# Kernel tuning notes

Measured on AMD Instinct MI355X. Metric: run time of the kernel, lower is better.

Reference implementation:

```python
import jax, jax.numpy as jnp
import numpy as np
from jax import lax

BN_EPS = 1e-5


def _conv(x, w, b):
    # 3x3 conv, stride 1, padding 1 (SAME), NCHW/OIHW
    y = lax.conv_general_dilated(x, w, (1, 1), 'SAME',
                                 dimension_numbers=('NCHW', 'OIHW', 'NCHW'))
    return y + b[None, :, None, None]


def _bn(x, g, b, m, v):
    # eval-mode batchnorm with running stats
    scale = (g / jnp.sqrt(v + BN_EPS))[None, :, None, None]
    return (x - m[None, :, None, None]) * scale + b[None, :, None, None]


def _pool(x):
    # MaxPool2d(2,2), VALID (floor division of spatial dims)
    return lax.reduce_window(x, -jnp.inf, lax.max, (1, 1, 2, 2), (1, 1, 2, 2), 'VALID')


def _quantum(xq, qp):
    """Batched 5-qubit statevector sim of the PennyLane circuit.
    Wire i: RX(xq[:, i%2]) then RY(qp[i%2]); CNOT(0,1); CNOT(1,2); <Z0 Z1>.
    xq: [B, 32] (only first 2 features used). Returns [B] float32.
    """
    B = xq.shape[0]
    psi = jnp.zeros((B, 32), jnp.complex64).at[:, 0].set(1.0)
    for i in range(5):  # fixed tiny loop over wires
        a = xq[:, i % 2]          # [B] data angle
        th = qp[i % 2]            # scalar weight angle
        ca, sa = jnp.cos(a * 0.5), jnp.sin(a * 0.5)
        RX = jnp.stack([jnp.stack([ca, -1j * sa], -1),
                        jnp.stack([-1j * sa, ca], -1)], -2).astype(jnp.complex64)  # [B,2,2]
        cb, sb = jnp.cos(th * 0.5), jnp.sin(th * 0.5)
        RY = jnp.stack([jnp.stack([cb, -sb]), jnp.stack([sb, cb])]).astype(jnp.complex64)  # [2,2]
        U = jnp.einsum('ij,bjk->bik', RY, RX)  # [B,2,2] per-wire unitary
        psi = psi.reshape(B, 2 ** i, 2, 2 ** (4 - i))
        psi = jnp.einsum('bij,bajc->baic', U, psi).reshape(B, 32)
    psi = psi.reshape(B, 2, 2, 2, 2, 2)
    # CNOT(0,1): flip qubit 1 where qubit 0 == 1
    psi = psi.at[:, 1].set(psi[:, 1, ::-1])
    # CNOT(1,2): flip qubit 2 where qubit 1 == 1
    psi = psi.at[:, :, 1].set(psi[:, :, 1, ::-1])
    z01 = jnp.array([[1.0, -1.0], [-1.0, 1.0]], jnp.float32).reshape(1, 2, 2, 1, 1, 1)
    prob = jnp.real(psi) ** 2 + jnp.imag(psi) ** 2
    return jnp.sum(prob * z01, axis=(1, 2, 3, 4, 5))


def setup_inputs() -> dict:
    key = jax.random.key(0)
    ks = jax.random.split(key, 24)
    B = 8192
    s = 0.05
    d = {}
    d['x'] = jax.random.normal(ks[0], (B, 1, 28, 28), jnp.float32)
    d['conv1_w'] = jax.random.normal(ks[1], (64, 1, 3, 3), jnp.float32) * s
    d['conv1_b'] = jax.random.normal(ks[2], (64,), jnp.float32) * s
    d['conv2_w'] = jax.random.normal(ks[3], (128, 64, 3, 3), jnp.float32) * s
    d['conv2_b'] = jax.random.normal(ks[4], (128,), jnp.float32) * s
    d['conv3_w'] = jax.random.normal(ks[5], (256, 128, 3, 3), jnp.float32) * s
    d['conv3_b'] = jax.random.normal(ks[6], (256,), jnp.float32) * s
    for i, c in [(1, 64), (2, 128), (3, 256)]:
        d[f'bn{i}_g'] = jnp.ones((c,), jnp.float32)
        d[f'bn{i}_b'] = jnp.zeros((c,), jnp.float32)
        d[f'bn{i}_m'] = jax.random.normal(ks[6 + i], (c,), jnp.float32) * 0.1
        d[f'bn{i}_v'] = jax.random.uniform(ks[9 + i], (c,), jnp.float32, 0.5, 1.5)
    d['fc1_w'] = jax.random.normal(ks[13], (32, 256 * 3 * 3), jnp.float32) * s
    d['fc1_b'] = jax.random.normal(ks[14], (32,), jnp.float32) * s
    d['q_params'] = jax.random.uniform(ks[15], (8,), jnp.float32)
    d['fc2_w'] = jax.random.normal(ks[16], (128, 1), jnp.float32) * s
    d['fc2_b'] = jax.random.normal(ks[17], (128,), jnp.float32) * s
    d['fc3_w'] = jax.random.normal(ks[18], (2, 128), jnp.float32) * s
    d['fc3_b'] = jax.random.normal(ks[19], (2,), jnp.float32) * s
    return d


def reference(x, conv1_w, conv1_b, conv2_w, conv2_b, conv3_w, conv3_b,
              bn1_g, bn1_b, bn1_m, bn1_v, bn2_g, bn2_b, bn2_m, bn2_v,
              bn3_g, bn3_b, bn3_m, bn3_v, fc1_w, fc1_b, q_params,
              fc2_w, fc2_b, fc3_w, fc3_b):
    h = _pool(jax.nn.relu(_bn(_conv(x, conv1_w, conv1_b), bn1_g, bn1_b, bn1_m, bn1_v)))
    h = _pool(jax.nn.relu(_bn(_conv(h, conv2_w, conv2_b), bn2_g, bn2_b, bn2_m, bn2_v)))
    h = _pool(jax.nn.relu(_bn(_conv(h, conv3_w, conv3_b), bn3_g, bn3_b, bn3_m, bn3_v)))
    # dropout is identity in eval mode
    h = h.reshape(h.shape[0], -1)              # [B, 2304]
    h = h @ fc1_w.T + fc1_b                     # [B, 32]
    q = _quantum(h, q_params)[:, None]          # [B, 1]
    h = q @ fc2_w.T + fc2_b                     # [B, 128]
    logits = h @ fc3_w.T + fc3_b                # [B, 2]
    return jax.nn.log_softmax(logits, axis=1)
```

## Files before the change

### kernel.cpp

```cpp
#include <hip/hip_runtime.h>
#include <hip/hip_bf16.h>
#include <math.h>

typedef float f32x4 __attribute__((ext_vector_type(4)));
typedef short s16x8 __attribute__((ext_vector_type(8)));

static const long long OFF_W2  = 0LL;
static const long long OFF_W3  = 147456LL;
static const long long OFF_AB1 = 737280LL;
static const long long OFF_AB2 = 737792LL;
static const long long OFF_AB3 = 738816LL;
static const long long OFF_Q   = 740864LL;

__device__ inline unsigned short f2bfu(float f) {
    __hip_bfloat16 h = __float2bfloat16(f);
    unsigned short u;
    __builtin_memcpy(&u, &h, 2);
    return u;
}

__global__ __launch_bounds__(256) void prep_k(
    const float* __restrict__ c2w, const float* __restrict__ c3w,
    const float* __restrict__ c1b, const float* __restrict__ g1, const float* __restrict__ b1,
    const float* __restrict__ m1, const float* __restrict__ v1,
    const float* __restrict__ c2b, const float* __restrict__ g2, const float* __restrict__ b2,
    const float* __restrict__ m2, const float* __restrict__ v2,
    const float* __restrict__ c3b, const float* __restrict__ g3, const float* __restrict__ b3,
    const float* __restrict__ m3, const float* __restrict__ v3,
    const float* __restrict__ fc1b, const float* __restrict__ qp,
    const float* __restrict__ fc2w, const float* __restrict__ fc2b,
    const float* __restrict__ fc3w, const float* __restrict__ fc3b,
    short* __restrict__ wT2, short* __restrict__ wT3,
    float2* __restrict__ ab1, float2* __restrict__ ab2, float2* __restrict__ ab3,
    float* __restrict__ qc)
{
    int tid = blockIdx.x * 256 + threadIdx.x;
    if (tid < 73728) {
        int ic = tid & 63, oc = (tid >> 6) & 127, k = tid >> 13;
        wT2[tid] = (short)f2bfu(c2w[(oc * 64 + ic) * 9 + k]);
    }
    if (tid < 294912) {
        int ic = tid & 127, oc = (tid >> 7) & 255, k = tid >> 15;
        wT3[tid] = (short)f2bfu(c3w[(oc * 128 + ic) * 9 + k]);
    }
    if (tid < 64) {
        float s = g1[tid] / sqrtf(v1[tid] + 1e-5f);
        ab1[tid] = make_float2(s, (c1b[tid] - m1[tid]) * s + b1[tid]);
    } else if (tid < 192) {
        int c = tid - 64;
        float s = g2[c] / sqrtf(v2[c] + 1e-5f);
        ab2[c] = make_float2(s, (c2b[c] - m2[c]) * s + b2[c]);
    } else if (tid < 448) {
        int c = tid - 192;
        float s = g3[c] / sqrtf(v3[c] + 1e-5f);
        ab3[c] = make_float2(s, (c3b[c] - m3[c]) * s + b3[c]);
    } else if (tid == 448) {
        float A0 = 0.f, A1 = 0.f, B0 = 0.f, B1 = 0.f;
        for (int k = 0; k < 128; ++k) {
            float f2 = fc2w[k], fb = fc2b[k];
            A0 += fc3w[k] * f2;        B0 += fc3w[k] * fb;
            A1 += fc3w[128 + k] * f2;  B1 += fc3w[128 + k] * fb;
        }
        qc[0] = A0; qc[1] = A1;
        qc[2] = B0 + fc3b[0]; qc[3] = B1 + fc3b[1];
        qc[4] = cosf(qp[1]);  qc[5] = fc1b[1];
    }
}

__global__ __launch_bounds__(256, 2) void fused_k(
    const float* __restrict__ x, const float* __restrict__ c1w,
    const float2* __restrict__ ab1, const float2* __restrict__ ab2,
    const float2* __restrict__ ab3,
    const short* __restrict__ wT2, const short* __restrict__ wT3,
    const float* __restrict__ fc1w, const float* __restrict__ qc,
    float* __restrict__ out)
{
    __shared__ float xt[30][32];
    __shared__ short xs2[16 * 16 * 64];
    __shared__ short xs3[8 * 8 * 128];
    __shared__ float red[4];

    int b = blockIdx.x, t = threadIdx.x;

    for (int i = t; i < 960;  i += 256) ((float*)xt)[i] = 0.f;
    for (int i = t; i < 8192; i += 256) ((unsigned*)xs2)[i] = 0u;
    for (int i = t; i < 4096; i += 256) ((unsigned*)xs3)[i] = 0u;
    __syncthreads();

    for (int i = t; i < 784; i += 256) xt[i / 28 + 1][i % 28 + 1] = x[b * 784 + i];

    int ocg = t & 7;
    float wr[8][9];
    float2 abr[8];
#pragma unroll
    for (int c = 0; c < 8; ++c) {
#pragma unroll
        for (int k = 0; k < 9; ++k) wr[c][k] = c1w[(ocg * 8 + c) * 9 + k];
        abr[c] = ab1[ocg * 8 + c];
    }
    __syncthreads();

    int posb = t >> 3;
    for (int p = posb; p < 196; p += 32) {
        int py = p / 14, px = p % 14;
        int y0 = 2 * py, x0 = 2 * px;
        float patch[4][4];
#pragma unroll
        for (int i = 0; i < 4; ++i)
#pragma unroll
            for (int j = 0; j < 4; ++j) patch[i][j] = xt[y0 + i][x0 + j];

        unsigned short ub[8];
#pragma unroll
        for (int c = 0; c < 8; ++c) {
            float a00 = 0.f, a01 = 0.f, a10 = 0.f, a11 = 0.f;
#pragma unroll
            for (int ky = 0; ky < 3; ++ky)
#pragma unroll
                for (int kx = 0; kx < 3; ++kx) {
                    float wv = wr[c][ky * 3 + kx];
                    a00 += patch[ky + 0][kx + 0] * wv;
                    a01 += patch[ky + 0][kx + 1] * wv;
                    a10 += patch[ky + 1][kx + 0] * wv;
                    a11 += patch[ky + 1][kx + 1] * wv;
                }
            float aa = abr[c].x, bb = abr[c].y;
            float v = fmaxf(fmaxf(a00 * aa + bb, a01 * aa + bb),
                            fmaxf(a10 * aa + bb, a11 * aa + bb));
            ub[c] = f2bfu(fmaxf(v, 0.f));
        }
        uint4 pk;
        pk.x = (unsigned)ub[0] | ((unsigned)ub[1] << 16);
        pk.y = (unsigned)ub[2] | ((unsigned)ub[3] << 16);
        pk.z = (unsigned)ub[4] | ((unsigned)ub[5] << 16);
        pk.w = (unsigned)ub[6] | ((unsigned)ub[7] << 16);
        int blk = ocg ^ ((px + 1) & 7);
        *(uint4*)&xs2[((((py + 1) * 16) + (px + 1)) * 8 + blk) * 8] = pk;
    }
    __syncthreads();

    int lane = t & 63, wid = t >> 6;
    int quad = lane >> 4, n16 = lane & 15;
    int dy = n16 >> 3, lx = n16 & 7;

    {
        f32x4 acc0[14], acc1[14];
        f32x4 z = {0.f, 0.f, 0.f, 0.f};
#pragma unroll
        for (int nt = 0; nt < 14; ++nt) { acc0[nt] = z; acc1[nt] = z; }

#pragma unroll 1
        for (int kykx = 0; kykx < 9; ++kykx) {
            int ky = kykx / 3, kx = kykx - 3 * ky;
            int dyky = dy + ky;
            int xc0 = lx + kx;
            int xc1 = xc0 + 8; if (xc1 > 15) xc1 = 15;
#pragma unroll
            for (int kk = 0; kk < 2; ++kk) {
                s16x8 A0 = *(const s16x8*)(wT2 + ((kykx * 128 + (wid * 2 + 0) * 16 + n16) * 64 + kk * 32 + quad * 8));
                s16x8 A1 = *(const s16x8*)(wT2 + ((kykx * 128 + (wid * 2 + 1) * 16 + n16) * 64 + kk * 32 + quad * 8));
                int bi = kk * 4 + quad;
#pragma unroll
                for (int nt = 0; nt < 14; ++nt) {
                    int ry = nt >> 1, cb = nt & 1;
                    int y_in = 2 * ry + dyky;
                    int x_in = cb ? xc1 : xc0;
                    int blk = bi ^ (x_in & 7);
                    s16x8 B = *(const s16x8*)&xs2[((y_in * 16 + x_in) * 8 + blk) * 8];
                    acc0[nt] = __builtin_amdgcn_mfma_f32_16x16x32_bf16(A0, B, acc0[nt], 0, 0, 0);
                    acc1[nt] = __builtin_amdgcn_mfma_f32_16x16x32_bf16(A1, B, acc1[nt], 0, 0, 0);
                }
            }
        }

        int m = lx >> 1;
        bool keep = (dy == 0) && ((lx & 1) == 0);
#pragma unroll
        for (int ml = 0; ml < 2; ++ml) {
            int oc0 = (wid * 2 + ml) * 16 + quad * 4;
            float2 abv[4];
#pragma unroll
            for (int r = 0; r < 4; ++r) abv[r] = ab2[oc0 + r];
#pragma unroll
            for (int nt = 0; nt < 14; ++nt) {
                int ry = nt >> 1, cb = nt & 1;
                int xp = cb * 4 + m;
                float pv[4];
#pragma unroll
                for (int r = 0; r < 4; ++r) {
                    float v = (ml ? acc1[nt][r] : acc0[nt][r]) * abv[r].x + abv[r].y;
                    v = fmaxf(v, __shfl_xor(v, 1));
                    v = fmaxf(v, __shfl_xor(v, 8));
                    pv[r] = fmaxf(v, 0.f);
                }
                if (keep && xp < 7) {
                    uint2 pk;
                    pk.x = (unsigned)f2bfu(pv[0]) | ((unsigned)f2bfu(pv[1]) << 16);
                    pk.y = (unsigned)f2bfu(pv[2]) | ((unsigned)f2bfu(pv[3]) << 16);
                    int blk3 = (oc0 >> 3) ^ (((xp + 1) & 7) << 1);
                    *(uint2*)&xs3[(((ry + 1) * 8 + (xp + 1)) * 16 + blk3) * 8 + (oc0 & 7)] = pk;
                }
            }
        }
    }
    __syncthreads();

    f32x4 acc[4][3];
    f32x4 z = {0.f, 0.f, 0.f, 0.f};
#pragma unroll
    for (int ml = 0; ml < 4; ++ml)
#pragma unroll
        for (int nt = 0; nt < 3; ++nt) acc[ml][nt] = z;

#pragma unroll 1
    for (int kykx = 0; kykx < 9; ++kykx) {
        int ky = kykx / 3, kx = kykx - 3 * ky;
        int dyky = dy + ky;
        int x_in = lx + kx; if (x_in > 7) x_in = 7;
#pragma unroll
        for (int kk = 0; kk < 4; ++kk) {
            s16x8 A[4];
#pragma unroll
            for (int ml = 0; ml < 4; ++ml)
                A[ml] = *(const s16x8*)(wT3 + ((kykx * 256 + (wid * 4 + ml) * 16 + n16) * 128 + kk * 32 + quad * 8));
            int bi = kk * 4 + quad;
            int blk = bi ^ ((x_in & 7) << 1);
#pragma unroll
            for (int nt = 0; nt < 3; ++nt) {
                int y_in = 2 * nt + dyky;
                s16x8 B = *(const s16x8*)&xs3[((y_in * 8 + x_in) * 16 + blk) * 8];
#pragma unroll
                for (int ml = 0; ml < 4; ++ml)
                    acc[ml][nt] = __builtin_amdgcn_mfma_f32_16x16x32_bf16(A[ml], B, acc[ml][nt], 0, 0, 0);
            }
        }
    }

    float vacc = 0.f;
    int m = lx >> 1;
    bool keep = (dy == 0) && ((lx & 1) == 0) && (m < 3);
    const float* fc1w1 = fc1w + 2304;
#pragma unroll
    for (int ml = 0; ml < 4; ++ml) {
        int oc0 = (wid * 4 + ml) * 16 + quad * 4;
        float2 abv[4];
#pragma unroll
        for (int r = 0; r < 4; ++r) abv[r] = ab3[oc0 + r];
#pragma unroll
        for (int nt = 0; nt < 3; ++nt) {
#pragma unroll
            for (int r = 0; r < 4; ++r) {
                float v = acc[ml][nt][r] * abv[r].x + abv[r].y;
                v = fmaxf(v, __shfl_xor(v, 1));
                v = fmaxf(v, __shfl_xor(v, 8));
                v = fmaxf(v, 0.f);
                if (keep) vacc += v * fc1w1[(oc0 + r) * 9 + nt * 3 + m];
            }
        }
    }
#pragma unroll
    for (int s = 1; s < 64; s <<= 1) vacc += __shfl_xor(vacc, s);
    if (lane == 0) red[wid] = vacc;
    __syncthreads();
    if (t == 0) {
        float v = red[0] + red[1] + red[2] + red[3] + qc[5];
        float q = cosf(v) * qc[4];
        float l0 = q * qc[0] + qc[2];
        float l1 = q * qc[1] + qc[3];
        float mx = fmaxf(l0, l1);
        float lse = mx + logf(__expf(l0 - mx) + __expf(l1 - mx));
        out[b * 2 + 0] = l0 - lse;
        out[b * 2 + 1] = l1 - lse;
    }
}

extern "C" void kernel_launch(void* const* d_in, const int* in_sizes, int n_in,
                              void* d_out, int out_size, void* d_ws, size_t ws_size,
                              hipStream_t stream)
{
    const float* x    = (const float*)d_in[0];
    const float* c1w  = (const float*)d_in[1];
    const float* c1b  = (const float*)d_in[2];
    const float* c2w  = (const float*)d_in[3];
    const float* c2b  = (const float*)d_in[4];
    const float* c3w  = (const float*)d_in[5];
    const float* c3b  = (const float*)d_in[6];
    const float* g1   = (const float*)d_in[7];
    const float* b1   = (const float*)d_in[8];
    const float* m1   = (const float*)d_in[9];
    const float* v1   = (const float*)d_in[10];
    const float* g2   = (const float*)d_in[11];
    const float* b2   = (const float*)d_in[12];
    const float* m2   = (const float*)d_in[13];
    const float* v2   = (const float*)d_in[14];
    const float* g3   = (const float*)d_in[15];
    const float* b3   = (const float*)d_in[16];
    const float* m3   = (const float*)d_in[17];
    const float* v3   = (const float*)d_in[18];
    const float* fc1w = (const float*)d_in[19];
    const float* fc1b = (const float*)d_in[20];
    const float* qp   = (const float*)d_in[21];
    const float* fc2w = (const float*)d_in[22];
    const float* fc2b = (const float*)d_in[23];
    const float* fc3w = (const float*)d_in[24];
    const float* fc3b = (const float*)d_in[25];
    float* out = (float*)d_out;
    char* ws = (char*)d_ws;

    short*  wT2 = (short*)(ws + OFF_W2);
    short*  wT3 = (short*)(ws + OFF_W3);
    float2* ab1 = (float2*)(ws + OFF_AB1);
    float2* ab2 = (float2*)(ws + OFF_AB2);
    float2* ab3 = (float2*)(ws + OFF_AB3);
    float*  qc  = (float*)(ws + OFF_Q);

    int B = in_sizes[0] / 784;

    prep_k<<<1152, 256, 0, stream>>>(c2w, c3w, c1b, g1, b1, m1, v1,
                                     c2b, g2, b2, m2, v2, c3b, g3, b3, m3, v3,
                                     fc1b, qp, fc2w, fc2b, fc3w, fc3b,
                                     wT2, wT3, ab1, ab2, ab3, qc);
    fused_k<<<B, 256, 0, stream>>>(x, c1w, ab1, ab2, ab3, wT2, wT3, fc1w, qc, out);
}
```

Measured before the change: 987.2 us.

## Alias conv2/conv3 LDS buffers, retile MFMA work per wave, raise occupancy

Merges the conv2 and conv3 LDS staging buffers into one aliased buffer that is re-zeroed between stages, cutting shared memory per block so launch bounds can request 3 blocks per SM. Conv2 is retiled so each wave owns one column half and 64 output channels, reusing 4 A fragments across 7 B loads. Conv3 is split by output-channel half and row group, which leaves an uneven 2-vs-1 tile split between waves. Conv1 uses packed float2 math. The risks are register pressure from the tighter bound and load imbalance in conv3.

Result: slower. 2.219 ms (+124.7%).

```diff
diff --git a/kernel.cpp b/kernel.cpp
--- a/kernel.cpp
+++ b/kernel.cpp
@@ -4,6 +4,7 @@
 
 typedef float f32x4 __attribute__((ext_vector_type(4)));
 typedef short s16x8 __attribute__((ext_vector_type(8)));
+typedef float v2f   __attribute__((ext_vector_type(2)));
 
 static const long long OFF_W2  = 0LL;
 static const long long OFF_W3  = 147456LL;
@@ -67,7 +68,7 @@
     }
 }
 
-__global__ __launch_bounds__(256, 2) void fused_k(
+__global__ __launch_bounds__(256, 3) void fused_k(
     const float* __restrict__ x, const float* __restrict__ c1w,
     const float2* __restrict__ ab1, const float2* __restrict__ ab2,
     const float2* __restrict__ ab3,
@@ -75,16 +76,14 @@
     const float* __restrict__ fc1w, const float* __restrict__ qc,
     float* __restrict__ out)
 {
+    __shared__ short smem[16 * 16 * 64 + 128];
     __shared__ float xt[30][32];
-    __shared__ short xs2[16 * 16 * 64];
-    __shared__ short xs3[8 * 8 * 128];
     __shared__ float red[4];
 
     int b = blockIdx.x, t = threadIdx.x;
 
+    for (int i = t; i < 8256; i += 256) ((unsigned*)smem)[i] = 0u;
     for (int i = t; i < 960;  i += 256) ((float*)xt)[i] = 0.f;
-    for (int i = t; i < 8192; i += 256) ((unsigned*)xs2)[i] = 0u;
-    for (int i = t; i < 4096; i += 256) ((unsigned*)xs3)[i] = 0u;
     __syncthreads();
 
     for (int i = t; i < 784; i += 256) xt[i / 28 + 1][i % 28 + 1] = x[b * 784 + i];
@@ -104,30 +103,31 @@
     for (int p = posb; p < 196; p += 32) {
         int py = p / 14, px = p % 14;
         int y0 = 2 * py, x0 = 2 * px;
-        float patch[4][4];
-#pragma unroll
-        for (int i = 0; i < 4; ++i)
-#pragma unroll
-            for (int j = 0; j < 4; ++j) patch[i][j] = xt[y0 + i][x0 + j];
-
+        v2f rowv[4][2];
+#pragma unroll
+        for (int i = 0; i < 4; ++i) {
+            rowv[i][0] = *(const v2f*)&xt[y0 + i][x0];
+            rowv[i][1] = *(const v2f*)&xt[y0 + i][x0 + 2];
+        }
         unsigned short ub[8];
 #pragma unroll
         for (int c = 0; c < 8; ++c) {
-            float a00 = 0.f, a01 = 0.f, a10 = 0.f, a11 = 0.f;
-#pragma unroll
-            for (int ky = 0; ky < 3; ++ky)
-#pragma unroll
-                for (int kx = 0; kx < 3; ++kx) {
-                    float wv = wr[c][ky * 3 + kx];
-                    a00 += patch[ky + 0][kx + 0] * wv;
-                    a01 += patch[ky + 0][kx + 1] * wv;
-                    a10 += patch[ky + 1][kx + 0] * wv;
-                    a11 += patch[ky + 1][kx + 1] * wv;
-                }
+            v2f a0 = {0.f, 0.f}, a1 = {0.f, 0.f};
+#pragma unroll
+            for (int ky = 0; ky < 3; ++ky) {
+                float w0 = wr[c][ky * 3 + 0], w1 = wr[c][ky * 3 + 1], w2 = wr[c][ky * 3 + 2];
+                v2f p00 = rowv[ky][0],     p01 = rowv[ky][1];
+                v2f p10 = rowv[ky + 1][0], p11 = rowv[ky + 1][1];
+                v2f q0; q0.x = p00.y; q0.y = p01.x;
+                v2f q1; q1.x = p10.y; q1.y = p11.x;
+                a0 += p00 * w0; a0 += q0 * w1; a0 += p01 * w2;
+                a1 += p10 * w0; a1 += q1 * w1; a1 += p11 * w2;
+            }
             float aa = abr[c].x, bb = abr[c].y;
-            float v = fmaxf(fmaxf(a00 * aa + bb, a01 * aa + bb),
-                            fmaxf(a10 * aa + bb, a11 * aa + bb));
-            ub[c] = f2bfu(fmaxf(v, 0.f));
+            v2f r0 = a0 * aa + bb;
+            v2f r1 = a1 * aa + bb;
+            float v = fmaxf(fmaxf(fmaxf(r0.x, r0.y), fmaxf(r1.x, r1.y)), 0.f);
+            ub[c] = f2bfu(v);
         }
         uint4 pk;
         pk.x = (unsigned)ub[0] | ((unsigned)ub[1] << 16);
@@ -135,126 +135,157 @@
         pk.z = (unsigned)ub[4] | ((unsigned)ub[5] << 16);
         pk.w = (unsigned)ub[6] | ((unsigned)ub[7] << 16);
         int blk = ocg ^ ((px + 1) & 7);
-        *(uint4*)&xs2[((((py + 1) * 16) + (px + 1)) * 8 + blk) * 8] = pk;
+        *(uint4*)&smem[((((py + 1) * 16) + (px + 1)) * 8 + blk) * 8] = pk;
     }
     __syncthreads();
 
     int lane = t & 63, wid = t >> 6;
     int quad = lane >> 4, n16 = lane & 15;
     int dy = n16 >> 3, lx = n16 & 7;
+    int cb = wid >> 1;
+    int oh = wid & 1;
 
     {
-        f32x4 acc0[14], acc1[14];
+        f32x4 acc[4][7];
         f32x4 z = {0.f, 0.f, 0.f, 0.f};
 #pragma unroll
-        for (int nt = 0; nt < 14; ++nt) { acc0[nt] = z; acc1[nt] = z; }
+        for (int ml = 0; ml < 4; ++ml)
+#pragma unroll
+            for (int ry = 0; ry < 7; ++ry) acc[ml][ry] = z;
 
 #pragma unroll 1
         for (int kykx = 0; kykx < 9; ++kykx) {
             int ky = kykx / 3, kx = kykx - 3 * ky;
-            int dyky = dy + ky;
-            int xc0 = lx + kx;
-            int xc1 = xc0 + 8; if (xc1 > 15) xc1 = 15;
+            int y0 = dy + ky;
+            int xc = lx + kx + cb * 8;
+            const short* aB = wT2 + (kykx * 128 + oh * 64 + n16) * 64 + quad * 8;
 #pragma unroll
             for (int kk = 0; kk < 2; ++kk) {
-                s16x8 A0 = *(const s16x8*)(wT2 + ((kykx * 128 + (wid * 2 + 0) * 16 + n16) * 64 + kk * 32 + quad * 8));
-                s16x8 A1 = *(const s16x8*)(wT2 + ((kykx * 128 + (wid * 2 + 1) * 16 + n16) * 64 + kk * 32 + quad * 8));
-                int bi = kk * 4 + quad;
-#pragma unroll
-                for (int nt = 0; nt < 14; ++nt) {
-                    int ry = nt >> 1, cb = nt & 1;
-                    int y_in = 2 * ry + dyky;
-                    int x_in = cb ? xc1 : xc0;
-                    int blk = bi ^ (x_in & 7);
-                    s16x8 B = *(const s16x8*)&xs2[((y_in * 16 + x_in) * 8 + blk) * 8];
-                    acc0[nt] = __builtin_amdgcn_mfma_f32_16x16x32_bf16(A0, B, acc0[nt], 0, 0, 0);
-                    acc1[nt] = __builtin_amdgcn_mfma_f32_16x16x32_bf16(A1, B, acc1[nt], 0, 0, 0);
-                }
-            }
-        }
+                int blk = (kk * 4 + quad) ^ (xc & 7);
+                const short* bp = &smem[((y0 * 16 + xc) * 8 + blk) * 8];
+                s16x8 A[4];
+#pragma unroll
+                for (int ml = 0; ml < 4; ++ml)
+                    A[ml] = *(const s16x8*)(aB + ml * 1024 + kk * 32);
+#pragma unroll
+                for (int ry = 0; ry < 7; ++ry) {
+                    s16x8 B = *(const s16x8*)(bp + ry * 2048);
+#pragma unroll
+                    for (int ml = 0; ml < 4; ++ml)
+                        acc[ml][ry] = __builtin_amdgcn_mfma_f32_16x16x32_bf16(A[ml], B, acc[ml][ry], 0, 0, 0);
+                }
+            }
+        }
+
+        __syncthreads();
+        for (int i = t; i < 4224; i += 256) ((unsigned*)smem)[i] = 0u;
+        __syncthreads();
 
         int m = lx >> 1;
-        bool keep = (dy == 0) && ((lx & 1) == 0);
-#pragma unroll
-        for (int ml = 0; ml < 2; ++ml) {
-            int oc0 = (wid * 2 + ml) * 16 + quad * 4;
+        int xp = cb * 4 + m;
+        bool keep = (dy == 0) && ((lx & 1) == 0) && (xp < 7);
+#pragma unroll
+        for (int ml = 0; ml < 4; ++ml) {
+            int oc0 = oh * 64 + ml * 16 + quad * 4;
             float2 abv[4];
 #pragma unroll
             for (int r = 0; r < 4; ++r) abv[r] = ab2[oc0 + r];
 #pragma unroll
-            for (int nt = 0; nt < 14; ++nt) {
-                int ry = nt >> 1, cb = nt & 1;
-                int xp = cb * 4 + m;
+            for (int ry = 0; ry < 7; ++ry) {
                 float pv[4];
 #pragma unroll
                 for (int r = 0; r < 4; ++r) {
-                    float v = (ml ? acc1[nt][r] : acc0[nt][r]) * abv[r].x + abv[r].y;
+                    float v = acc[ml][ry][r] * abv[r].x + abv[r].y;
                     v = fmaxf(v, __shfl_xor(v, 1));
                     v = fmaxf(v, __shfl_xor(v, 8));
                     pv[r] = fmaxf(v, 0.f);
                 }
-                if (keep && xp < 7) {
+                if (keep) {
                     uint2 pk;
                     pk.x = (unsigned)f2bfu(pv[0]) | ((unsigned)f2bfu(pv[1]) << 16);
                     pk.y = (unsigned)f2bfu(pv[2]) | ((unsigned)f2bfu(pv[3]) << 16);
                     int blk3 = (oc0 >> 3) ^ (((xp + 1) & 7) << 1);
-                    *(uint2*)&xs3[(((ry + 1) * 8 + (xp + 1)) * 16 + blk3) * 8 + (oc0 & 7)] = pk;
-                }
-            }
-        }
-    }
-    __syncthreads();
-
-    f32x4 acc[4][3];
-    f32x4 z = {0.f, 0.f, 0.f, 0.f};
-#pragma unroll
-    for (int ml = 0; ml < 4; ++ml)
-#pragma unroll
-        for (int nt = 0; nt < 3; ++nt) acc[ml][nt] = z;
-
+                    *(uint2*)&smem[(((ry + 1) * 8 + (xp + 1)) * 16 + blk3) * 8 + (oc0 & 7)] = pk;
+                }
+            }
+        }
+    }
+    __syncthreads();
+
+    int oh3 = wid & 1;
+    int nth = wid >> 1;
+
+    f32x4 acc3[8][2];
+    {
+        f32x4 z = {0.f, 0.f, 0.f, 0.f};
+#pragma unroll
+        for (int ml = 0; ml < 8; ++ml) { acc3[ml][0] = z; acc3[ml][1] = z; }
+    }
+
+    if (nth == 0) {
 #pragma unroll 1
-    for (int kykx = 0; kykx < 9; ++kykx) {
-        int ky = kykx / 3, kx = kykx - 3 * ky;
-        int dyky = dy + ky;
-        int x_in = lx + kx; if (x_in > 7) x_in = 7;
-#pragma unroll
-        for (int kk = 0; kk < 4; ++kk) {
-            s16x8 A[4];
-#pragma unroll
-            for (int ml = 0; ml < 4; ++ml)
-                A[ml] = *(const s16x8*)(wT3 + ((kykx * 256 + (wid * 4 + ml) * 16 + n16) * 128 + kk * 32 + quad * 8));
-            int bi = kk * 4 + quad;
-            int blk = bi ^ ((x_in & 7) << 1);
-#pragma unroll
-            for (int nt = 0; nt < 3; ++nt) {
-                int y_in = 2 * nt + dyky;
-                s16x8 B = *(const s16x8*)&xs3[((y_in * 8 + x_in) * 16 + blk) * 8];
-#pragma unroll
-                for (int ml = 0; ml < 4; ++ml)
-                    acc[ml][nt] = __builtin_amdgcn_mfma_f32_16x16x32_bf16(A[ml], B, acc[ml][nt], 0, 0, 0);
+        for (int kykx = 0; kykx < 9; ++kykx) {
+            int ky = kykx / 3, kx = kykx - 3 * ky;
+            int y0 = dy + ky;
+            int x0 = lx + kx;
+            const short* aB = wT3 + (kykx * 256 + oh3 * 128 + n16) * 128 + quad * 8;
+#pragma unroll
+            for (int kk = 0; kk < 4; ++kk) {
+                int blk = (kk * 4 + quad) ^ ((x0 & 7) << 1);
+                const short* bp = &smem[((y0 * 8 + x0) * 16 + blk) * 8];
+                s16x8 B0 = *(const s16x8*)(bp);
+                s16x8 B1 = *(const s16x8*)(bp + 2048);
+#pragma unroll
+                for (int ml = 0; ml < 8; ++ml) {
+                    s16x8 A = *(const s16x8*)(aB + ml * 2048 + kk * 32);
+                    acc3[ml][0] = __builtin_amdgcn_mfma_f32_16x16x32_bf16(A, B0, acc3[ml][0], 0, 0, 0);
+                    acc3[ml][1] = __builtin_amdgcn_mfma_f32_16x16x32_bf16(A, B1, acc3[ml][1], 0, 0, 0);
+                }
+            }
+        }
+    } else {
+#pragma unroll 1
+        for (int kykx = 0; kykx < 9; ++kykx) {
+            int ky = kykx / 3, kx = kykx - 3 * ky;
+            int y0 = dy + ky;
+            int x0 = lx + kx;
+            const short* aB = wT3 + (kykx * 256 + oh3 * 128 + n16) * 128 + quad * 8;
+#pragma unroll
+            for (int kk = 0; kk < 4; ++kk) {
+                int blk = (kk * 4 + quad) ^ ((x0 & 7) << 1);
+                const short* bp = &smem[((y0 * 8 + x0) * 16 + blk) * 8 + 4096];
+                s16x8 B0 = *(const s16x8*)(bp);
+#pragma unroll
+                for (int ml = 0; ml < 8; ++ml) {
+                    s16x8 A = *(const s16x8*)(aB + ml * 2048 + kk * 32);
+                    acc3[ml][0] = __builtin_amdgcn_mfma_f32_16x16x32_bf16(A, B0, acc3[ml][0], 0, 0, 0);
+                }
             }
         }
     }
 
     float vacc = 0.f;
-    int m = lx >> 1;
-    bool keep = (dy == 0) && ((lx & 1) == 0) && (m < 3);
-    const float* fc1w1 = fc1w + 2304;
-#pragma unroll
-    for (int ml = 0; ml < 4; ++ml) {
-        int oc0 = (wid * 4 + ml) * 16 + quad * 4;
-        float2 abv[4];
-#pragma unroll
-        for (int r = 0; r < 4; ++r) abv[r] = ab3[oc0 + r];
-#pragma unroll
-        for (int nt = 0; nt < 3; ++nt) {
-#pragma unroll
-            for (int r = 0; r < 4; ++r) {
-                float v = acc[ml][nt][r] * abv[r].x + abv[r].y;
-                v = fmaxf(v, __shfl_xor(v, 1));
-                v = fmaxf(v, __shfl_xor(v, 8));
-                v = fmaxf(v, 0.f);
-                if (keep) vacc += v * fc1w1[(oc0 + r) * 9 + nt * 3 + m];
+    {
+        int m = lx >> 1;
+        bool keep = (dy == 0) && ((lx & 1) == 0) && (m < 3);
+        const float* fc1w1 = fc1w + 2304;
+        int ntCount = (nth == 0) ? 2 : 1;
+#pragma unroll
+        for (int ml = 0; ml < 8; ++ml) {
+            int oc0 = oh3 * 128 + ml * 16 + quad * 4;
+            float2 abv[4];
+#pragma unroll
+            for (int r = 0; r < 4; ++r) abv[r] = ab3[oc0 + r];
+            for (int ntl = 0; ntl < ntCount; ++ntl) {
+                int nt = nth * 2 + ntl;
+#pragma unroll
+                for (int r = 0; r < 4; ++r) {
+                    float v = acc3[ml][ntl][r] * abv[r].x + abv[r].y;
+                    v = fmaxf(v, __shfl_xor(v, 1));
+                    v = fmaxf(v, __shfl_xor(v, 8));
+                    v = fmaxf(v, 0.f);
+                    if (keep) vacc += v * fc1w1[(oc0 + r) * 9 + nt * 3 + m];
+                }
             }
         }
     }
```
